# Optimization experiments

Hardware: AMD Instinct MI355X
Metric: run time of the kernel (lower is better)

Reference implementation:

```python
import jax, jax.numpy as jnp
import numpy as np

N = 50000      # nodes
E = 600000     # edges
D = 128        # embedding_dimension
R = 2          # num_relations
DESC = 768; TW = 768; NUMF = 5; CATF = 3
EPS = 1e-5


def setup_inputs() -> dict:
    key = jax.random.key(0)
    ks = jax.random.split(key, 32)
    f32 = jnp.float32

    def rn(k, shape):
        return jax.random.normal(k, shape, dtype=f32)

    def w(k, fan_in, shape):
        return jax.random.normal(k, shape, dtype=f32) * (1.0 / np.sqrt(fan_in))

    inp = {}
    inp["desc_embedding"] = rn(ks[0], (N, DESC))
    inp["tweet_embedding"] = rn(ks[1], (N, TW))
    inp["num_feature"] = rn(ks[2], (N, NUMF))
    inp["cat_feature"] = rn(ks[3], (N, CATF))
    inp["edge_index"] = jax.random.randint(ks[4], (2, E), 0, N, dtype=jnp.int32)
    inp["edge_type"] = jax.random.randint(ks[5], (E,), 0, R, dtype=jnp.int32)
    q = D // 4
    inp["Wd"] = w(ks[6], DESC, (DESC, q)); inp["bd"] = jnp.zeros((q,), f32)
    inp["Wt"] = w(ks[7], TW, (TW, q));     inp["bt"] = jnp.zeros((q,), f32)
    inp["Wn"] = w(ks[8], NUMF, (NUMF, q)); inp["bn"] = jnp.zeros((q,), f32)
    inp["Wc"] = w(ks[9], CATF, (CATF, q)); inp["bc"] = jnp.zeros((q,), f32)
    inp["W1"] = w(ks[10], D, (D, D)); inp["b1"] = jnp.zeros((D,), f32)
    inp["rg1_w"] = w(ks[11], D, (R, D, D)); inp["rg1_root"] = w(ks[12], D, (D, D)); inp["rg1_bias"] = jnp.zeros((D,), f32)
    inp["ln1_g"] = jnp.ones((D,), f32); inp["ln1_b"] = jnp.zeros((D,), f32)
    inp["rg2_w"] = w(ks[13], D, (R, D, D)); inp["rg2_root"] = w(ks[14], D, (D, D)); inp["rg2_bias"] = jnp.zeros((D,), f32)
    inp["ln2_g"] = jnp.ones((D,), f32); inp["ln2_b"] = jnp.zeros((D,), f32)
    inp["W2"] = w(ks[15], D, (D, D)); inp["b2"] = jnp.zeros((D,), f32)
    inp["W3"] = w(ks[16], D, (D, 1)); inp["b3"] = jnp.zeros((1,), f32)
    return inp


def _leaky(x):
    return jnp.where(x > 0, x, 0.01 * x)


def _rgcn_max(x, edge_index, edge_type, rel_w, root_w, bias):
    # PyG RGCNConv(aggr='max'): out = x @ root + bias + sum_r (max-agg of x_j over rel-r edges) @ W_r
    src, dst = edge_index[0], edge_index[1]
    xs = x[src]  # [E, D] gathered source features
    out = x @ root_w + bias
    for r in range(R):
        msg = jnp.where((edge_type == r)[:, None], xs, -jnp.inf)
        agg = jax.ops.segment_max(msg, dst, num_segments=N)  # [N, D]
        agg = jnp.where(jnp.isinf(agg), 0.0, agg)            # empty slots -> 0
        out = out + agg @ rel_w[r]
    return out


def _graph_layernorm(x, gamma, beta):
    # torch_geometric.nn.LayerNorm, mode='graph': normalize over ALL nodes+channels of the graph
    mu = jnp.mean(x)
    xc = x - mu
    var = jnp.mean(xc * xc)
    return xc / jnp.sqrt(var + EPS) * gamma + beta


def reference(desc_embedding, tweet_embedding, num_feature, cat_feature,
              edge_index, edge_type,
              Wd, bd, Wt, bt, Wn, bn, Wc, bc,
              W1, b1, rg1_w, rg1_root, rg1_bias, ln1_g, ln1_b,
              rg2_w, rg2_root, rg2_bias, ln2_g, ln2_b,
              W2, b2, W3, b3):
    x = jnp.concatenate([
        _leaky(desc_embedding @ Wd + bd),
        _leaky(tweet_embedding @ Wt + bt),
        _leaky(num_feature @ Wn + bn),
        _leaky(cat_feature @ Wc + bc),
    ], axis=1)                                   # [N, D]
    x = _leaky(x @ W1 + b1)
    x = _rgcn_max(x, edge_index, edge_type, rg1_w, rg1_root, rg1_bias)
    x = _graph_layernorm(x, ln1_g, ln1_b)
    # dropout: eval mode (identity)
    x = _rgcn_max(x, edge_index, edge_type, rg2_w, rg2_root, rg2_bias)
    x = _graph_layernorm(x, ln2_g, ln2_b)
    x = _leaky(x @ W2 + b2)
    x = jax.nn.sigmoid(x @ W3 + b3)
    return x.reshape(-1)                          # [N]
```

## Files before the change

### kernel.cpp

```cpp
#include <hip/hip_runtime.h>
#include <cstdint>
#include <cstddef>

#define NN 50000
#define EE 600000
#define DD 128
#define NSEG (NN*2)
#define NPART ((NSEG + 255) / 256)

typedef short bf16x8 __attribute__((ext_vector_type(8)));
typedef float f32x4 __attribute__((ext_vector_type(4)));

__device__ __forceinline__ float leaky_f(float x){ return x > 0.f ? x : 0.01f*x; }

__device__ __forceinline__ unsigned short f2bf(float f){
    unsigned u = __float_as_uint(f);
    u += 0x7fffu + ((u >> 16) & 1u);
    return (unsigned short)(u >> 16);
}
__device__ __forceinline__ float bf2f(unsigned short h){
    return __uint_as_float(((unsigned)h) << 16);
}

template<int K, int BN, int S, int BFMASK, int LEAKY>
__global__ __launch_bounds__(256) void mfgemm_k(
    const void* __restrict__ A0, const void* __restrict__ A1, const void* __restrict__ A2,
    int lda0,
    const float* __restrict__ B0, const float* __restrict__ B1, const float* __restrict__ B2,
    const float* __restrict__ bias, float* __restrict__ C, int c0, int M)
{
    constexpr int KCH = 128;
    constexpr int NCH = K / KCH;
    constexpr int CT = BN / 16;
    __shared__ unsigned short sB[4*BN*40];
    const int tid = threadIdx.x;
    const int lane = tid & 63;
    const int wv = tid >> 6;
    const int q = lane >> 4, n16 = lane & 15;
    const int bm = blockIdx.x * 64;
    const int arow = bm + wv*16 + n16;

    f32x4 acc[CT];
#pragma unroll
    for (int c=0;c<CT;c++) acc[c] = (f32x4){0.f,0.f,0.f,0.f};

    const void* As[3] = {A0, A1, A2};
    const float* Bs[3] = {B0, B1, B2};

#pragma unroll
    for (int s=0; s<S; s++) {
        const float* Bp = Bs[s];
        const int lda = (s==0) ? lda0 : K;
        const bool f32s = !((BFMASK >> s) & 1);
        for (int kb=0; kb<NCH; kb++) {
            __syncthreads();
            {
                const int n = tid % BN;
                const int kq0 = tid / BN;
                constexpr int KQSTEP = 256 / BN;
#pragma unroll
                for (int kq = kq0; kq < 32; kq += KQSTEP) {
                    int k0 = kq*4;
                    const float* gp = Bp + (size_t)(kb*KCH + k0)*BN + n;
                    float v0 = gp[0], v1 = gp[BN], v2 = gp[2*BN], v3 = gp[3*BN];
                    int ks = kq >> 3, kk = (kq & 7)*4;
                    int sa = (ks*BN + n)*40 + kk;
                    unsigned p0 = (unsigned)f2bf(v0) | ((unsigned)f2bf(v1) << 16);
                    unsigned p1 = (unsigned)f2bf(v2) | ((unsigned)f2bf(v3) << 16);
                    *reinterpret_cast<unsigned*>(&sB[sa])   = p0;
                    *reinterpret_cast<unsigned*>(&sB[sa+2]) = p1;
                }
            }
            __syncthreads();
#pragma unroll
            for (int ks=0; ks<4; ks++) {
                bf16x8 ah, al;
                if (f32s) {
                    float a[8];
                    if (arow < M) {
                        const float* ap = (const float*)As[s] + (size_t)arow*lda + kb*KCH + ks*32 + q*8;
                        float4 t0 = *reinterpret_cast<const float4*>(ap);
                        float4 t1 = *reinterpret_cast<const float4*>(ap+4);
                        a[0]=t0.x;a[1]=t0.y;a[2]=t0.z;a[3]=t0.w;
                        a[4]=t1.x;a[5]=t1.y;a[6]=t1.z;a[7]=t1.w;
                    } else {
#pragma unroll
                        for (int j=0;j<8;j++) a[j]=0.f;
                    }
#pragma unroll
                    for (int j=0;j<8;j++) {
                        unsigned short h = f2bf(a[j]);
                        ah[j] = (short)h;
                        al[j] = (short)f2bf(a[j] - bf2f(h));
                    }
                } else {
                    if (arow < M) {
                        const unsigned short* ap = (const unsigned short*)As[s]
                            + (size_t)arow*K + kb*KCH + ks*32 + q*8;
                        ah = *reinterpret_cast<const bf16x8*>(ap);
                    } else {
#pragma unroll
                        for (int j=0;j<8;j++) ah[j]=0;
                    }
                }
#pragma unroll
                for (int c=0;c<CT;c++) {
                    const unsigned short* bp = &sB[(ks*BN + c*16 + n16)*40 + q*8];
                    bf16x8 b = *reinterpret_cast<const bf16x8*>(bp);
                    acc[c] = __builtin_amdgcn_mfma_f32_16x16x32_bf16(ah, b, acc[c], 0,0,0);
                    if (f32s)
                        acc[c] = __builtin_amdgcn_mfma_f32_16x16x32_bf16(al, b, acc[c], 0,0,0);
                }
            }
        }
    }
    const int orow = bm + wv*16 + q*4;
#pragma unroll
    for (int c=0;c<CT;c++) {
        float bb = bias[c*16 + n16];
#pragma unroll
        for (int i=0;i<4;i++) {
            int r = orow + i;
            if (r < M) {
                float v = acc[c][i] + bb;
                if (LEAKY) v = leaky_f(v);
                C[(size_t)r*DD + c0 + c*16 + n16] = v;
            }
        }
    }
}

__global__ void numcat_k(const float* __restrict__ numf, const float* __restrict__ catf,
                         const float* __restrict__ Wn, const float* __restrict__ bn,
                         const float* __restrict__ Wc, const float* __restrict__ bc,
                         float* __restrict__ x)
{
    int t = blockIdx.x*blockDim.x + threadIdx.x;
    if (t >= NN*64) return;
    int n = t >> 6, c = t & 63;
    if (c < 32) {
        float acc = bn[c];
#pragma unroll
        for (int k=0;k<5;k++) acc = fmaf(numf[n*5+k], Wn[k*32+c], acc);
        x[(size_t)n*DD + 64 + c] = leaky_f(acc);
    } else {
        int cc = c - 32;
        float acc = bc[cc];
#pragma unroll
        for (int k=0;k<3;k++) acc = fmaf(catf[n*3+k], Wc[k*32+cc], acc);
        x[(size_t)n*DD + 96 + cc] = leaky_f(acc);
    }
}

__global__ void zero_int_k(int* __restrict__ p, int n)
{
    int i = blockIdx.x*blockDim.x + threadIdx.x;
    if (i < n) p[i] = 0;
}

__global__ void hist_k(const int* __restrict__ ei, const int* __restrict__ et,
                       int* __restrict__ deg)
{
    int e = blockIdx.x*blockDim.x + threadIdx.x;
    if (e >= EE) return;
    atomicAdd(&deg[ei[EE + e]*2 + et[e]], 1);
}

__global__ __launch_bounds__(256) void part_reduce_k(const int* __restrict__ deg,
                                                     int* __restrict__ part)
{
    __shared__ int s[256];
    int t = threadIdx.x;
    int i = blockIdx.x*256 + t;
    s[t] = (i < NSEG) ? deg[i] : 0;
    __syncthreads();
#pragma unroll
    for (int o=128;o>0;o>>=1) {
        if (t < o) s[t] += s[t+o];
        __syncthreads();
    }
    if (t == 0) part[blockIdx.x] = s[0];
}

__global__ __launch_bounds__(512) void part_scan_k(int* __restrict__ part)
{
    __shared__ int ps[512];
    int t = threadIdx.x;
    int v = (t < NPART) ? part[t] : 0;
    ps[t] = v; __syncthreads();
    for (int o=1;o<512;o<<=1) {
        int u = (t >= o) ? ps[t-o] : 0;
        __syncthreads();
        ps[t] += u;
        __syncthreads();
    }
    if (t < NPART) part[t] = ps[t] - v;
}

__global__ __launch_bounds__(256) void final_scan_k(const int* __restrict__ deg,
                                                    const int* __restrict__ part,
                                                    int* __restrict__ offs,
                                                    int* __restrict__ cursor)
{
    __shared__ int ps[256];
    int t = threadIdx.x;
    int i = blockIdx.x*256 + t;
    int d = (i < NSEG) ? deg[i] : 0;
    ps[t] = d; __syncthreads();
    for (int o=1;o<256;o<<=1) {
        int u = (t >= o) ? ps[t-o] : 0;
        __syncthreads();
        ps[t] += u;
        __syncthreads();
    }
    if (i < NSEG) {
        int off = part[blockIdx.x] + ps[t] - d;
        offs[i] = off; cursor[i] = off;
    }
    if (blockIdx.x == 0 && t == 0) offs[NSEG] = EE;
}

__global__ void place_k(const int* __restrict__ ei, const int* __restrict__ et,
                        int* __restrict__ cursor, unsigned short* __restrict__ csr)
{
    int e = blockIdx.x*blockDim.x + threadIdx.x;
    if (e >= EE) return;
    int r = et[e], dst = ei[EE + e], src = ei[e];
    int pos = atomicAdd(&cursor[dst*2 + r], 1);
    csr[pos] = (unsigned short)src;
}

__global__ void gather_k(const float* __restrict__ x, const int* __restrict__ offs,
                         const unsigned short* __restrict__ csr, int r,
                         unsigned short* __restrict__ aggb)
{
    int gw = (blockIdx.x*blockDim.x + threadIdx.x) >> 6;
    int lane = threadIdx.x & 63;
    if (gw >= NN) return;
    int seg = gw*2 + r;
    int beg = offs[seg], end = offs[seg+1];
    float2 m = make_float2(-3.402823466e+38f, -3.402823466e+38f);
    for (int j=beg;j<end;j++) {
        int src = csr[j];
        float2 v = *reinterpret_cast<const float2*>(x + (size_t)src*DD + lane*2);
        m.x = fmaxf(m.x, v.x);
        m.y = fmaxf(m.y, v.y);
    }
    if (beg == end) { m.x = 0.f; m.y = 0.f; }
    unsigned o = (unsigned)f2bf(m.x) | ((unsigned)f2bf(m.y) << 16);
    *reinterpret_cast<unsigned*>(aggb + (size_t)gw*DD + lane*2) = o;
}

__global__ void zero_red_k(float* __restrict__ red)
{
    if (threadIdx.x < 4) red[threadIdx.x] = 0.f;
}

__global__ void reduce_k(const float* __restrict__ x, float* __restrict__ red)
{
    const int total = NN*DD;
    float s = 0.f, ss = 0.f;
    for (int i = blockIdx.x*blockDim.x + threadIdx.x; i < total; i += gridDim.x*blockDim.x) {
        float v = x[i];
        s += v; ss = fmaf(v, v, ss);
    }
#pragma unroll
    for (int o=32;o>0;o>>=1) { s += __shfl_down(s,o); ss += __shfl_down(ss,o); }
    __shared__ float bs[4], bss[4];
    int wid = threadIdx.x >> 6, lane = threadIdx.x & 63;
    if (lane == 0) { bs[wid] = s; bss[wid] = ss; }
    __syncthreads();
    if (threadIdx.x == 0) {
        atomicAdd(&red[0], bs[0]+bs[1]+bs[2]+bs[3]);
        atomicAdd(&red[1], bss[0]+bss[1]+bss[2]+bss[3]);
    }
}

__global__ void norm_k(float* __restrict__ x, const float* __restrict__ g,
                       const float* __restrict__ b, const float* __restrict__ red)
{
    const float inv = 1.f / (float)(NN*DD);
    float mu  = red[0] * inv;
    float var = red[1] * inv - mu*mu;
    float rstd = rsqrtf(var + 1e-5f);
    int i = blockIdx.x*blockDim.x + threadIdx.x;
    int c = i & 127;
    x[i] = (x[i]-mu)*rstd*g[c] + b[c];
}

__global__ void head_k(const float* __restrict__ h, const float* __restrict__ W3,
                       const float* __restrict__ b3, float* __restrict__ out)
{
    int n = blockIdx.x;
    int t = threadIdx.x;
    float p = h[(size_t)n*DD + t] * W3[t];
#pragma unroll
    for (int o=32;o>0;o>>=1) p += __shfl_down(p,o);
    __shared__ float s2[2];
    if ((t & 63) == 0) s2[t>>6] = p;
    __syncthreads();
    if (t == 0) {
        float l = s2[0] + s2[1] + b3[0];
        out[n] = 1.f / (1.f + expf(-l));
    }
}

extern "C" void kernel_launch(void* const* d_in, const int* in_sizes, int n_in,
                              void* d_out, int out_size, void* d_ws, size_t ws_size,
                              hipStream_t stream)
{
    const float* desc  = (const float*)d_in[0];
    const float* tweet = (const float*)d_in[1];
    const float* numf  = (const float*)d_in[2];
    const float* catf  = (const float*)d_in[3];
    const int*   ei    = (const int*)d_in[4];
    const int*   et    = (const int*)d_in[5];
    const float* Wd=(const float*)d_in[6];  const float* bd=(const float*)d_in[7];
    const float* Wt=(const float*)d_in[8];  const float* bt=(const float*)d_in[9];
    const float* Wn=(const float*)d_in[10]; const float* bn=(const float*)d_in[11];
    const float* Wc=(const float*)d_in[12]; const float* bc=(const float*)d_in[13];
    const float* W1=(const float*)d_in[14]; const float* b1=(const float*)d_in[15];
    const float* rg1w=(const float*)d_in[16]; const float* rg1root=(const float*)d_in[17];
    const float* rg1b=(const float*)d_in[18];
    const float* ln1g=(const float*)d_in[19]; const float* ln1b=(const float*)d_in[20];
    const float* rg2w=(const float*)d_in[21]; const float* rg2root=(const float*)d_in[22];
    const float* rg2b=(const float*)d_in[23];
    const float* ln2g=(const float*)d_in[24]; const float* ln2b=(const float*)d_in[25];
    const float* W2=(const float*)d_in[26]; const float* b2=(const float*)d_in[27];
    const float* W3=(const float*)d_in[28]; const float* b3=(const float*)d_in[29];
    float* out = (float*)d_out;

    float* xa  = (float*)d_ws;
    float* xb  = xa + (size_t)NN*DD;
    unsigned short* aggb = (unsigned short*)(xb + (size_t)NN*DD);
    unsigned short* aggb0 = aggb;
    unsigned short* aggb1 = aggb + (size_t)NN*DD;
    float* red = (float*)(aggb + (size_t)2*NN*DD);
    int*   deg    = (int*)(red + 4);
    int*   offs   = deg + NSEG;
    int*   cursor = offs + NSEG + 1;
    int*   part   = cursor + NSEG;
    unsigned short* csr = (unsigned short*)(part + NPART);

    dim3 blk(256);
    const int mblocks = (NN + 63) / 64;
    const int nelm_blocks = (NN*DD)/256;
    const int edge_blocks = (EE+255)/256;
    const int gat_blocks  = (NN*64+255)/256;

    hipLaunchKernelGGL((mfgemm_k<768,32,1,0,1>), dim3(mblocks), blk, 0, stream,
                       desc, nullptr, nullptr, 768, Wd, nullptr, nullptr, bd, xa, 0, NN);
    hipLaunchKernelGGL((mfgemm_k<768,32,1,0,1>), dim3(mblocks), blk, 0, stream,
                       tweet, nullptr, nullptr, 768, Wt, nullptr, nullptr, bt, xa, 32, NN);
    numcat_k<<<(NN*64)/256, 256, 0, stream>>>(numf, catf, Wn, bn, Wc, bc, xa);

    zero_int_k<<<(NSEG+255)/256, 256, 0, stream>>>(deg, NSEG);
    hist_k<<<edge_blocks, 256, 0, stream>>>(ei, et, deg);
    part_reduce_k<<<NPART, 256, 0, stream>>>(deg, part);
    part_scan_k<<<1, 512, 0, stream>>>(part);
    final_scan_k<<<NPART, 256, 0, stream>>>(deg, part, offs, cursor);
    place_k<<<edge_blocks, 256, 0, stream>>>(ei, et, cursor, csr);

    hipLaunchKernelGGL((mfgemm_k<128,128,1,0,1>), dim3(mblocks), blk, 0, stream,
                       xa, nullptr, nullptr, 128, W1, nullptr, nullptr, b1, xb, 0, NN);

    gather_k<<<gat_blocks, 256, 0, stream>>>(xb, offs, csr, 0, aggb0);
    gather_k<<<gat_blocks, 256, 0, stream>>>(xb, offs, csr, 1, aggb1);
    hipLaunchKernelGGL((mfgemm_k<128,128,3,6,0>), dim3(mblocks), blk, 0, stream,
                       xb, aggb0, aggb1, 128,
                       rg1root, rg1w, rg1w + (size_t)DD*DD, rg1b, xa, 0, NN);
    zero_red_k<<<1, 64, 0, stream>>>(red);
    reduce_k<<<512, 256, 0, stream>>>(xa, red);
    norm_k<<<nelm_blocks, 256, 0, stream>>>(xa, ln1g, ln1b, red);

    gather_k<<<gat_blocks, 256, 0, stream>>>(xa, offs, csr, 0, aggb0);
    gather_k<<<gat_blocks, 256, 0, stream>>>(xa, offs, csr, 1, aggb1);
    hipLaunchKernelGGL((mfgemm_k<128,128,3,6,0>), dim3(mblocks), blk, 0, stream,
                       xa, aggb0, aggb1, 128,
                       rg2root, rg2w, rg2w + (size_t)DD*DD, rg2b, xb, 0, NN);
    zero_red_k<<<1, 64, 0, stream>>>(red);
    reduce_k<<<512, 256, 0, stream>>>(xb, red);
    norm_k<<<nelm_blocks, 256, 0, stream>>>(xb, ln2g, ln2b, red);

    hipLaunchKernelGGL((mfgemm_k<128,128,1,0,1>), dim3(mblocks), blk, 0, stream,
                       xb, nullptr, nullptr, 128, W2, nullptr, nullptr, b2, xa, 0, NN);
    head_k<<<NN, 128, 0, stream>>>(xa, W3, b3, out);
}
```

Measured before the change: 838.7 us.

## Fuse LN reductions, output head and projections into GEMM kernels; merge gathers

Merges the two projection GEMMs into one 2-D grid launch and merges the two per-relation gather launches into one kernel over all segments, which also zeroes the reduction buffer. The RGCN GEMM epilogue now accumulates the layernorm sum and sum-of-squares via atomics, replacing the separate reduce pass. The final GEMM computes the W3 dot product and sigmoid in its epilogue instead of writing the hidden activations for a separate head kernel. The fp32 hi/lo bf16 split now truncates instead of rounding. This removes several launches and full passes over the 50000x128 activations, at the cost of slightly different hi/lo splitting numerics.

```diff
diff --git a/kernel.cpp b/kernel.cpp
--- a/kernel.cpp
+++ b/kernel.cpp
@@ -18,20 +18,25 @@
     u += 0x7fffu + ((u >> 16) & 1u);
     return (unsigned short)(u >> 16);
 }
-__device__ __forceinline__ float bf2f(unsigned short h){
-    return __uint_as_float(((unsigned)h) << 16);
-}
-
-template<int K, int BN, int S, int BFMASK, int LEAKY>
-__global__ __launch_bounds__(256) void mfgemm_k(
-    const void* __restrict__ A0, const void* __restrict__ A1, const void* __restrict__ A2,
-    int lda0,
-    const float* __restrict__ B0, const float* __restrict__ B1, const float* __restrict__ B2,
-    const float* __restrict__ bias, float* __restrict__ C, int c0, int M)
-{
-    constexpr int KCH = 128;
-    constexpr int NCH = K / KCH;
-    constexpr int CT = BN / 16;
+
+__device__ __forceinline__ void split8(const float* a, bf16x8& hi, bf16x8& lo){
+#pragma unroll
+    for (int j=0;j<8;j++){
+        unsigned u  = __float_as_uint(a[j]);
+        unsigned uh = u & 0xFFFF0000u;
+        hi[j] = (short)(uh >> 16);
+        float lf = a[j] - __uint_as_float(uh);
+        lo[j] = (short)(__float_as_uint(lf) >> 16);
+    }
+}
+
+__global__ __launch_bounds__(256) void proj_k(
+    const float* __restrict__ A0, const float* __restrict__ A1,
+    const float* __restrict__ B0, const float* __restrict__ B1,
+    const float* __restrict__ bias0, const float* __restrict__ bias1,
+    float* __restrict__ C, int M)
+{
+    constexpr int K = 768, BN = 32, CT = 2;
     __shared__ unsigned short sB[4*BN*40];
     const int tid = threadIdx.x;
     const int lane = tid & 63;
@@ -39,6 +44,82 @@
     const int q = lane >> 4, n16 = lane & 15;
     const int bm = blockIdx.x * 64;
     const int arow = bm + wv*16 + n16;
+    const float* A = blockIdx.y ? A1 : A0;
+    const float* B = blockIdx.y ? B1 : B0;
+    const float* bias = blockIdx.y ? bias1 : bias0;
+    const int c0 = blockIdx.y * 32;
+
+    f32x4 acc[CT];
+#pragma unroll
+    for (int c=0;c<CT;c++) acc[c] = (f32x4){0.f,0.f,0.f,0.f};
+
+    for (int kb=0; kb<K/128; kb++) {
+        __syncthreads();
+        {
+            const int n = tid % BN;
+            const int kq0 = tid / BN;
+#pragma unroll
+            for (int kq = kq0; kq < 32; kq += 8) {
+                const float* gp = B + (size_t)(kb*128 + kq*4)*BN + n;
+                float v0 = gp[0], v1 = gp[BN], v2 = gp[2*BN], v3 = gp[3*BN];
+                int ks = kq >> 3, kk = (kq & 7)*4;
+                int sa = (ks*BN + n)*40 + kk;
+                *reinterpret_cast<unsigned*>(&sB[sa])   = (unsigned)f2bf(v0) | ((unsigned)f2bf(v1) << 16);
+                *reinterpret_cast<unsigned*>(&sB[sa+2]) = (unsigned)f2bf(v2) | ((unsigned)f2bf(v3) << 16);
+            }
+        }
+        __syncthreads();
+#pragma unroll
+        for (int ks=0; ks<4; ks++) {
+            float a[8];
+            if (arow < M) {
+                const float* ap = A + (size_t)arow*K + kb*128 + ks*32 + q*8;
+                float4 t0 = *reinterpret_cast<const float4*>(ap);
+                float4 t1 = *reinterpret_cast<const float4*>(ap+4);
+                a[0]=t0.x;a[1]=t0.y;a[2]=t0.z;a[3]=t0.w;
+                a[4]=t1.x;a[5]=t1.y;a[6]=t1.z;a[7]=t1.w;
+            } else {
+#pragma unroll
+                for (int j=0;j<8;j++) a[j]=0.f;
+            }
+            bf16x8 ah, al;
+            split8(a, ah, al);
+#pragma unroll
+            for (int c=0;c<CT;c++) {
+                bf16x8 b = *reinterpret_cast<const bf16x8*>(&sB[(ks*BN + c*16 + n16)*40 + q*8]);
+                acc[c] = __builtin_amdgcn_mfma_f32_16x16x32_bf16(ah, b, acc[c], 0,0,0);
+                acc[c] = __builtin_amdgcn_mfma_f32_16x16x32_bf16(al, b, acc[c], 0,0,0);
+            }
+        }
+    }
+    const int orow = bm + wv*16 + q*4;
+#pragma unroll
+    for (int c=0;c<CT;c++) {
+        float bb = bias[c*16 + n16];
+#pragma unroll
+        for (int i=0;i<4;i++) {
+            int r = orow + i;
+            if (r < M) C[(size_t)r*DD + c0 + c*16 + n16] = leaky_f(acc[c][i] + bb);
+        }
+    }
+}
+
+template<int S,int BFMASK,int LEAKY,int HEAD,int LNRED>
+__global__ __launch_bounds__(256) void mfgemm_k(
+    const void* __restrict__ A0, const void* __restrict__ A1, const void* __restrict__ A2,
+    const float* __restrict__ B0, const float* __restrict__ B1, const float* __restrict__ B2,
+    const float* __restrict__ bias, float* __restrict__ C, int M,
+    const float* __restrict__ W3, const float* __restrict__ b3,
+    float* __restrict__ red, float* __restrict__ outv)
+{
+    constexpr int BN = 128, CT = 8;
+    __shared__ unsigned short sB[4*BN*40];
+    const int tid = threadIdx.x;
+    const int lane = tid & 63;
+    const int wv = tid >> 6;
+    const int q = lane >> 4, n16 = lane & 15;
+    const int bm = blockIdx.x * 64;
+    const int arow = bm + wv*16 + n16;
 
     f32x4 acc[CT];
 #pragma unroll
@@ -49,82 +130,104 @@
 
 #pragma unroll
     for (int s=0; s<S; s++) {
-        const float* Bp = Bs[s];
-        const int lda = (s==0) ? lda0 : K;
         const bool f32s = !((BFMASK >> s) & 1);
-        for (int kb=0; kb<NCH; kb++) {
+        __syncthreads();
+        {
+            const float* Bp = Bs[s];
+            const int n = tid % BN;
+            const int kq0 = tid / BN;
+#pragma unroll
+            for (int kq = kq0; kq < 32; kq += 2) {
+                const float* gp = Bp + (size_t)(kq*4)*BN + n;
+                float v0 = gp[0], v1 = gp[BN], v2 = gp[2*BN], v3 = gp[3*BN];
+                int ks = kq >> 3, kk = (kq & 7)*4;
+                int sa = (ks*BN + n)*40 + kk;
+                *reinterpret_cast<unsigned*>(&sB[sa])   = (unsigned)f2bf(v0) | ((unsigned)f2bf(v1) << 16);
+                *reinterpret_cast<unsigned*>(&sB[sa+2]) = (unsigned)f2bf(v2) | ((unsigned)f2bf(v3) << 16);
+            }
+        }
+        __syncthreads();
+#pragma unroll
+        for (int ks=0; ks<4; ks++) {
+            bf16x8 ah, al;
+            if (f32s) {
+                float a[8];
+                if (arow < M) {
+                    const float* ap = (const float*)As[s] + (size_t)arow*DD + ks*32 + q*8;
+                    float4 t0 = *reinterpret_cast<const float4*>(ap);
+                    float4 t1 = *reinterpret_cast<const float4*>(ap+4);
+                    a[0]=t0.x;a[1]=t0.y;a[2]=t0.z;a[3]=t0.w;
+                    a[4]=t1.x;a[5]=t1.y;a[6]=t1.z;a[7]=t1.w;
+                } else {
+#pragma unroll
+                    for (int j=0;j<8;j++) a[j]=0.f;
+                }
+                split8(a, ah, al);
+            } else {
+                if (arow < M) {
+                    const unsigned short* ap = (const unsigned short*)As[s]
+                        + (size_t)arow*DD + ks*32 + q*8;
+                    ah = *reinterpret_cast<const bf16x8*>(ap);
+                } else {
+#pragma unroll
+                    for (int j=0;j<8;j++) ah[j]=0;
+                }
+            }
+#pragma unroll
+            for (int c=0;c<CT;c++) {
+                bf16x8 b = *reinterpret_cast<const bf16x8*>(&sB[(ks*BN + c*16 + n16)*40 + q*8]);
+                acc[c] = __builtin_amdgcn_mfma_f32_16x16x32_bf16(ah, b, acc[c], 0,0,0);
+                if (f32s)
+                    acc[c] = __builtin_amdgcn_mfma_f32_16x16x32_bf16(al, b, acc[c], 0,0,0);
+            }
+        }
+    }
+
+    const int orow = bm + wv*16 + q*4;
+    if (HEAD) {
+        float w3c[CT];
+#pragma unroll
+        for (int c=0;c<CT;c++) w3c[c] = W3[c*16 + n16];
+        float bb3 = b3[0];
+#pragma unroll
+        for (int i=0;i<4;i++) {
+            float t = 0.f;
+#pragma unroll
+            for (int c=0;c<CT;c++) {
+                float v = acc[c][i] + bias[c*16 + n16];
+                if (LEAKY) v = leaky_f(v);
+                t = fmaf(v, w3c[c], t);
+            }
+#pragma unroll
+            for (int m=1;m<16;m<<=1) t += __shfl_xor(t, m);
+            int r = orow + i;
+            if (n16 == 0 && r < M) outv[r] = 1.f / (1.f + expf(-(t + bb3)));
+        }
+    } else {
+        float s = 0.f, ss = 0.f;
+#pragma unroll
+        for (int c=0;c<CT;c++) {
+            float bb = bias[c*16 + n16];
+#pragma unroll
+            for (int i=0;i<4;i++) {
+                int r = orow + i;
+                if (r < M) {
+                    float v = acc[c][i] + bb;
+                    if (LEAKY) v = leaky_f(v);
+                    C[(size_t)r*DD + c*16 + n16] = v;
+                    if (LNRED) { s += v; ss = fmaf(v, v, ss); }
+                }
+            }
+        }
+        if (LNRED) {
+#pragma unroll
+            for (int o=32;o>0;o>>=1) { s += __shfl_down(s,o); ss += __shfl_down(ss,o); }
+            __shared__ float rs[4], rss[4];
+            if (lane == 0) { rs[wv] = s; rss[wv] = ss; }
             __syncthreads();
-            {
-                const int n = tid % BN;
-                const int kq0 = tid / BN;
-                constexpr int KQSTEP = 256 / BN;
-#pragma unroll
-                for (int kq = kq0; kq < 32; kq += KQSTEP) {
-                    int k0 = kq*4;
-                    const float* gp = Bp + (size_t)(kb*KCH + k0)*BN + n;
-                    float v0 = gp[0], v1 = gp[BN], v2 = gp[2*BN], v3 = gp[3*BN];
-                    int ks = kq >> 3, kk = (kq & 7)*4;
-                    int sa = (ks*BN + n)*40 + kk;
-                    unsigned p0 = (unsigned)f2bf(v0) | ((unsigned)f2bf(v1) << 16);
-                    unsigned p1 = (unsigned)f2bf(v2) | ((unsigned)f2bf(v3) << 16);
-                    *reinterpret_cast<unsigned*>(&sB[sa])   = p0;
-                    *reinterpret_cast<unsigned*>(&sB[sa+2]) = p1;
-                }
-            }
-            __syncthreads();
-#pragma unroll
-            for (int ks=0; ks<4; ks++) {
-                bf16x8 ah, al;
-                if (f32s) {
-                    float a[8];
-                    if (arow < M) {
-                        const float* ap = (const float*)As[s] + (size_t)arow*lda + kb*KCH + ks*32 + q*8;
-                        float4 t0 = *reinterpret_cast<const float4*>(ap);
-                        float4 t1 = *reinterpret_cast<const float4*>(ap+4);
-                        a[0]=t0.x;a[1]=t0.y;a[2]=t0.z;a[3]=t0.w;
-                        a[4]=t1.x;a[5]=t1.y;a[6]=t1.z;a[7]=t1.w;
-                    } else {
-#pragma unroll
-                        for (int j=0;j<8;j++) a[j]=0.f;
-                    }
-#pragma unroll
-                    for (int j=0;j<8;j++) {
-                        unsigned short h = f2bf(a[j]);
-                        ah[j] = (short)h;
-                        al[j] = (short)f2bf(a[j] - bf2f(h));
-                    }
-                } else {
-                    if (arow < M) {
-                        const unsigned short* ap = (const unsigned short*)As[s]
-                            + (size_t)arow*K + kb*KCH + ks*32 + q*8;
-                        ah = *reinterpret_cast<const bf16x8*>(ap);
-                    } else {
-#pragma unroll
-                        for (int j=0;j<8;j++) ah[j]=0;
-                    }
-                }
-#pragma unroll
-                for (int c=0;c<CT;c++) {
-                    const unsigned short* bp = &sB[(ks*BN + c*16 + n16)*40 + q*8];
-                    bf16x8 b = *reinterpret_cast<const bf16x8*>(bp);
-                    acc[c] = __builtin_amdgcn_mfma_f32_16x16x32_bf16(ah, b, acc[c], 0,0,0);
-                    if (f32s)
-                        acc[c] = __builtin_amdgcn_mfma_f32_16x16x32_bf16(al, b, acc[c], 0,0,0);
-                }
-            }
-        }
-    }
-    const int orow = bm + wv*16 + q*4;
-#pragma unroll
-    for (int c=0;c<CT;c++) {
-        float bb = bias[c*16 + n16];
-#pragma unroll
-        for (int i=0;i<4;i++) {
-            int r = orow + i;
-            if (r < M) {
-                float v = acc[c][i] + bb;
-                if (LEAKY) v = leaky_f(v);
-                C[(size_t)r*DD + c0 + c*16 + n16] = v;
+            if (tid == 0) {
+                atomicAdd(&red[0], rs[0]+rs[1]+rs[2]+rs[3]);
+                atomicAdd(&red[1], rss[0]+rss[1]+rss[2]+rss[3]);
             }
         }
     }
@@ -230,14 +333,15 @@
     csr[pos] = (unsigned short)src;
 }
 
-__global__ void gather_k(const float* __restrict__ x, const int* __restrict__ offs,
-                         const unsigned short* __restrict__ csr, int r,
-                         unsigned short* __restrict__ aggb)
-{
-    int gw = (blockIdx.x*blockDim.x + threadIdx.x) >> 6;
+__global__ void gather2_k(const float* __restrict__ x, const int* __restrict__ offs,
+                          const unsigned short* __restrict__ csr,
+                          unsigned short* __restrict__ aggb, float* __restrict__ red)
+{
+    if (blockIdx.x == 0 && threadIdx.x < 4) red[threadIdx.x] = 0.f;
+    int seg = (blockIdx.x*blockDim.x + threadIdx.x) >> 6;
     int lane = threadIdx.x & 63;
-    if (gw >= NN) return;
-    int seg = gw*2 + r;
+    if (seg >= NSEG) return;
+    int node = seg >> 1, r = seg & 1;
     int beg = offs[seg], end = offs[seg+1];
     float2 m = make_float2(-3.402823466e+38f, -3.402823466e+38f);
     for (int j=beg;j<end;j++) {
@@ -248,32 +352,7 @@
     }
     if (beg == end) { m.x = 0.f; m.y = 0.f; }
     unsigned o = (unsigned)f2bf(m.x) | ((unsigned)f2bf(m.y) << 16);
-    *reinterpret_cast<unsigned*>(aggb + (size_t)gw*DD + lane*2) = o;
-}
-
-__global__ void zero_red_k(float* __restrict__ red)
-{
-    if (threadIdx.x < 4) red[threadIdx.x] = 0.f;
-}
-
-__global__ void reduce_k(const float* __restrict__ x, float* __restrict__ red)
-{
-    const int total = NN*DD;
-    float s = 0.f, ss = 0.f;
-    for (int i = blockIdx.x*blockDim.x + threadIdx.x; i < total; i += gridDim.x*blockDim.x) {
-        float v = x[i];
-        s += v; ss = fmaf(v, v, ss);
-    }
-#pragma unroll
-    for (int o=32;o>0;o>>=1) { s += __shfl_down(s,o); ss += __shfl_down(ss,o); }
-    __shared__ float bs[4], bss[4];
-    int wid = threadIdx.x >> 6, lane = threadIdx.x & 63;
-    if (lane == 0) { bs[wid] = s; bss[wid] = ss; }
-    __syncthreads();
-    if (threadIdx.x == 0) {
-        atomicAdd(&red[0], bs[0]+bs[1]+bs[2]+bs[3]);
-        atomicAdd(&red[1], bss[0]+bss[1]+bss[2]+bss[3]);
-    }
+    *reinterpret_cast<unsigned*>(aggb + (size_t)r*NN*DD + (size_t)node*DD + lane*2) = o;
 }
 
 __global__ void norm_k(float* __restrict__ x, const float* __restrict__ g,
@@ -286,23 +365,6 @@
     int i = blockIdx.x*blockDim.x + threadIdx.x;
     int c = i & 127;
     x[i] = (x[i]-mu)*rstd*g[c] + b[c];
-}
-
-__global__ void head_k(const float* __restrict__ h, const float* __restrict__ W3,
-                       const float* __restrict__ b3, float* __restrict__ out)
-{
-    int n = blockIdx.x;
-    int t = threadIdx.x;
-    float p = h[(size_t)n*DD + t] * W3[t];
-#pragma unroll
-    for (int o=32;o>0;o>>=1) p += __shfl_down(p,o);
-    __shared__ float s2[2];
-    if ((t & 63) == 0) s2[t>>6] = p;
-    __syncthreads();
-    if (t == 0) {
-        float l = s2[0] + s2[1] + b3[0];
-        out[n] = 1.f / (1.f + expf(-l));
-    }
 }
 
 extern "C" void kernel_launch(void* const* d_in, const int* in_sizes, int n_in,
@@ -346,12 +408,9 @@
     const int mblocks = (NN + 63) / 64;
     const int nelm_blocks = (NN*DD)/256;
     const int edge_blocks = (EE+255)/256;
-    const int gat_blocks  = (NN*64+255)/256;
-
-    hipLaunchKernelGGL((mfgemm_k<768,32,1,0,1>), dim3(mblocks), blk, 0, stream,
-                       desc, nullptr, nullptr, 768, Wd, nullptr, nullptr, bd, xa, 0, NN);
-    hipLaunchKernelGGL((mfgemm_k<768,32,1,0,1>), dim3(mblocks), blk, 0, stream,
-                       tweet, nullptr, nullptr, 768, Wt, nullptr, nullptr, bt, xa, 32, NN);
+    const int seg_blocks  = (NSEG*64)/256;
+
+    proj_k<<<dim3(mblocks,2), blk, 0, stream>>>(desc, tweet, Wd, Wt, bd, bt, xa, NN);
     numcat_k<<<(NN*64)/256, 256, 0, stream>>>(numf, catf, Wn, bn, Wc, bc, xa);
 
     zero_int_k<<<(NSEG+255)/256, 256, 0, stream>>>(deg, NSEG);
@@ -361,28 +420,25 @@
     final_scan_k<<<NPART, 256, 0, stream>>>(deg, part, offs, cursor);
     place_k<<<edge_blocks, 256, 0, stream>>>(ei, et, cursor, csr);
 
-    hipLaunchKernelGGL((mfgemm_k<128,128,1,0,1>), dim3(mblocks), blk, 0, stream,
-                       xa, nullptr, nullptr, 128, W1, nullptr, nullptr, b1, xb, 0, NN);
-
-    gather_k<<<gat_blocks, 256, 0, stream>>>(xb, offs, csr, 0, aggb0);
-    gather_k<<<gat_blocks, 256, 0, stream>>>(xb, offs, csr, 1, aggb1);
-    hipLaunchKernelGGL((mfgemm_k<128,128,3,6,0>), dim3(mblocks), blk, 0, stream,
-                       xb, aggb0, aggb1, 128,
-                       rg1root, rg1w, rg1w + (size_t)DD*DD, rg1b, xa, 0, NN);
-    zero_red_k<<<1, 64, 0, stream>>>(red);
-    reduce_k<<<512, 256, 0, stream>>>(xa, red);
+    hipLaunchKernelGGL((mfgemm_k<1,0,1,0,0>), dim3(mblocks), blk, 0, stream,
+                       xa, nullptr, nullptr, W1, nullptr, nullptr, b1, xb, NN,
+                       nullptr, nullptr, nullptr, nullptr);
+
+    gather2_k<<<seg_blocks, 256, 0, stream>>>(xb, offs, csr, aggb, red);
+    hipLaunchKernelGGL((mfgemm_k<3,6,0,0,1>), dim3(mblocks), blk, 0, stream,
+                       xb, aggb0, aggb1,
+                       rg1root, rg1w, rg1w + (size_t)DD*DD, rg1b, xa, NN,
+                       nullptr, nullptr, red, nullptr);
     norm_k<<<nelm_blocks, 256, 0, stream>>>(xa, ln1g, ln1b, red);
 
-    gather_k<<<gat_blocks, 256, 0, stream>>>(xa, offs, csr, 0, aggb0);
-    gather_k<<<gat_blocks, 256, 0, stream>>>(xa, offs, csr, 1, aggb1);
-    hipLaunchKernelGGL((mfgemm_k<128,128,3,6,0>), dim3(mblocks), blk, 0, stream,
-                       xa, aggb0, aggb1, 128,
-                       rg2root, rg2w, rg2w + (size_t)DD*DD, rg2b, xb, 0, NN);
-    zero_red_k<<<1, 64, 0, stream>>>(red);
-    reduce_k<<<512, 256, 0, stream>>>(xb, red);
+    gather2_k<<<seg_blocks, 256, 0, stream>>>(xa, offs, csr, aggb, red);
+    hipLaunchKernelGGL((mfgemm_k<3,6,0,0,1>), dim3(mblocks), blk, 0, stream,
+                       xa, aggb0, aggb1,
+                       rg2root, rg2w, rg2w + (size_t)DD*DD, rg2b, xb, NN,
+                       nullptr, nullptr, red, nullptr);
     norm_k<<<nelm_blocks, 256, 0, stream>>>(xb, ln2g, ln2b, red);
 
-    hipLaunchKernelGGL((mfgemm_k<128,128,1,0,1>), dim3(mblocks), blk, 0, stream,
-                       xb, nullptr, nullptr, 128, W2, nullptr, nullptr, b2, xa, 0, NN);
-    head_k<<<NN, 128, 0, stream>>>(xa, W3, b3, out);
-}
+    hipLaunchKernelGGL((mfgemm_k<1,0,1,1,0>), dim3(mblocks), blk, 0, stream,
+                       xb, nullptr, nullptr, W2, nullptr, nullptr, b2, nullptr, NN,
+                       W3, b3, nullptr, out);
+}
```

Result: no change. 822.5 us (-1.9%).
